# Performance work log

Measured on AMD Instinct MI355X. Metric: run time of the kernel, lower is better.

Reference implementation:

```python
import jax, jax.numpy as jnp
import numpy as np

B, T, D = 4, 1024, 1024
H, DH = 16, 64
SCALE = 1.0 / (DH ** 0.5)


def skew(QE):
    # QE: [B, H, T, 2T-1] -> relative-position skew (Music Transformer)
    b, h, t, _ = QE.shape
    QE = jnp.pad(QE, ((0, 0), (0, 0), (0, 0), (0, 1))).reshape(b, h, 2 * t * t)
    QE = jnp.pad(QE, ((0, 0), (0, 0), (0, t - 1))).reshape(b, h, t + 1, 2 * t - 1)
    return QE[:, :, :t, -t:]


def setup_inputs() -> dict:
    key = jax.random.key(0)
    ks = jax.random.split(key, 11)
    s = 0.02
    return {
        "x": jax.random.normal(ks[0], (B, T, D), jnp.float32),
        "context": jax.random.normal(ks[1], (B, T, D), jnp.float32),
        "mask": jax.random.randint(ks[2], (B, 1, T, T), 0, 2).astype(jnp.bool_),
        "lookup_table": jax.random.normal(ks[3], (2 * T - 1, DH), jnp.float32) * s,
        "Wq": jax.random.normal(ks[4], (D, H * DH), jnp.float32) * s,
        "Wk": jax.random.normal(ks[5], (D, H * DH), jnp.float32) * s,
        "Wv": jax.random.normal(ks[6], (D, H * DH), jnp.float32) * s,
        "Wo": jax.random.normal(ks[7], (H * DH, D), jnp.float32) * s,
        "bo": jnp.zeros((D,), jnp.float32),
        "gamma": jnp.ones((D,), jnp.float32),
        "beta": jnp.zeros((D,), jnp.float32),
    }


def reference(x, context, mask, lookup_table, Wq, Wk, Wv, Wo, bo, gamma, beta):
    b, t, d = x.shape
    # projections -> [B, H, T, DH]
    q = (x @ Wq).reshape(b, t, H, DH).transpose(0, 2, 1, 3)
    k = (context @ Wk).reshape(b, t, H, DH).transpose(0, 2, 1, 3)
    v = (context @ Wv).reshape(b, t, H, DH).transpose(0, 2, 1, 3)

    score = jnp.einsum("bhqd,bhkd->bhqk", q, k)
    score = score + skew(jnp.einsum("bhqd,rd->bhqr", q, lookup_table))
    score = score * SCALE
    score = jnp.where(mask, jnp.float32(-1e9), score)
    attn = jax.nn.softmax(score, axis=-1)

    out = jnp.einsum("bhqk,bhkd->bhqd", attn, v)
    out = out.transpose(0, 2, 1, 3).reshape(b, t, H * DH)
    out = out @ Wo + bo  # dropout is identity at inference (p effectively 0)

    y = x + out
    mu = jnp.mean(y, axis=-1, keepdims=True)
    var = jnp.var(y, axis=-1, keepdims=True)
    return (y - mu) / jnp.sqrt(var + 1e-5) * gamma + beta
```

## Files before the change

### kernel.cpp

```cpp
#include <hip/hip_runtime.h>

#define Tn 1024
#define Hn 16
#define Dn 1024
#define DHn 64
#define QSCALE 0.18033688011112042f

typedef unsigned short u16;
typedef unsigned long long ull;
typedef __bf16 bf16x8 __attribute__((ext_vector_type(8)));
typedef float f32x4 __attribute__((ext_vector_type(4)));

__device__ __forceinline__ u16 f2bf(float f) {
  union { float f; unsigned u; } v; v.f = f;
  return (u16)((v.u + 0x7FFFu + ((v.u >> 16) & 1u)) >> 16);
}
__device__ __forceinline__ float bf2f(u16 s) {
  union { unsigned u; float f; } v; v.u = ((unsigned)s) << 16;
  return v.f;
}
__device__ __forceinline__ f32x4 mfma16(bf16x8 a, bf16x8 b, f32x4 c) {
  return __builtin_amdgcn_mfma_f32_16x16x32_bf16(a, b, c, 0, 0, 0);
}

__global__ void k_convert(const float* __restrict__ src, u16* __restrict__ dst, int n) {
  int i = (blockIdx.x * blockDim.x + threadIdx.x) * 4;
  if (i >= n) return;
  float4 v = *(const float4*)(src + i);
  union { u16 s[4]; uint2 u; } o;
  o.s[0] = f2bf(v.x); o.s[1] = f2bf(v.y); o.s[2] = f2bf(v.z); o.s[3] = f2bf(v.w);
  *(uint2*)(dst + i) = o.u;
}

__global__ __launch_bounds__(256) void k_maskpack(const unsigned char* __restrict__ m,
                                                  unsigned long long* __restrict__ mb) {
  int wi = blockIdx.x * 4 + (threadIdx.x >> 6);
  int lane = threadIdx.x & 63;
  unsigned char v = m[((size_t)wi << 6) + lane];
  unsigned long long bal = __ballot(v != 0);
  if (lane == 0) mb[wi] = bal;
}

__global__ void k_transpose_convert(const float* __restrict__ W, u16* __restrict__ Wt) {
  __shared__ float tile[32][33];
  int n0 = blockIdx.x * 32, k0 = blockIdx.y * 32;
  int tx = threadIdx.x, ty = threadIdx.y;
  #pragma unroll
  for (int i = 0; i < 4; i++)
    tile[ty + 8*i][tx] = W[(size_t)(k0 + ty + 8*i) * Dn + n0 + tx];
  __syncthreads();
  #pragma unroll
  for (int i = 0; i < 4; i++)
    Wt[(size_t)(n0 + ty + 8*i) * Dn + k0 + tx] = f2bf(tile[tx][ty + 8*i]);
}

__global__ __launch_bounds__(256) void k_proj(const float* __restrict__ x, const float* __restrict__ ctxI,
                                              const u16* __restrict__ WqT, const u16* __restrict__ WkvT,
                                              u16* __restrict__ Qb, u16* __restrict__ Kb, u16* __restrict__ Vb) {
  __shared__ __align__(16) u16 Al[128][40];
  __shared__ __align__(16) u16 Bl[128][40];
  int bx = blockIdx.x;
  bool isQ = bx < 256;
  int idx = isQ ? bx : bx - 256;
  int m0 = (idx & 31) * 128;
  int n0 = (idx >> 5) * 128;
  const float* A = isQ ? x : ctxI;
  const u16* Bt = isQ ? WqT : WkvT;
  u16* dst0 = isQ ? Qb : Kb;
  float scale = isQ ? QSCALE : 1.0f;
  int tid = threadIdx.x;
  int w = tid >> 6, lane = tid & 63, g = lane >> 4, lr = lane & 15;
  int wr = w >> 1, wc = w & 1;
  f32x4 acc[4][4] = {};
  int sr = tid >> 2, sc = tid & 3;
  const float* Ap0 = &A[(size_t)(m0 + sr) * Dn + sc * 8];
  const float* Ap1 = Ap0 + (size_t)64 * Dn;
  const u16* Bp0 = &Bt[(size_t)(n0 + sr) * Dn + sc * 8];
  const u16* Bp1 = Bp0 + (size_t)64 * Dn;
  float4 ra0a = *(const float4*)Ap0, ra0b = *(const float4*)(Ap0 + 4);
  float4 ra1a = *(const float4*)Ap1, ra1b = *(const float4*)(Ap1 + 4);
  int4 rb0 = *(const int4*)Bp0;
  int4 rb1 = *(const int4*)Bp1;
  for (int k0 = 0; k0 < Dn; k0 += 32) {
    __syncthreads();
    {
      union { u16 s[8]; int4 v; } c0, c1;
      c0.s[0]=f2bf(ra0a.x); c0.s[1]=f2bf(ra0a.y); c0.s[2]=f2bf(ra0a.z); c0.s[3]=f2bf(ra0a.w);
      c0.s[4]=f2bf(ra0b.x); c0.s[5]=f2bf(ra0b.y); c0.s[6]=f2bf(ra0b.z); c0.s[7]=f2bf(ra0b.w);
      c1.s[0]=f2bf(ra1a.x); c1.s[1]=f2bf(ra1a.y); c1.s[2]=f2bf(ra1a.z); c1.s[3]=f2bf(ra1a.w);
      c1.s[4]=f2bf(ra1b.x); c1.s[5]=f2bf(ra1b.y); c1.s[6]=f2bf(ra1b.z); c1.s[7]=f2bf(ra1b.w);
      *(int4*)&Al[sr][sc*8]      = c0.v;
      *(int4*)&Al[sr + 64][sc*8] = c1.v;
    }
    *(int4*)&Bl[sr][sc*8]      = rb0;
    *(int4*)&Bl[sr + 64][sc*8] = rb1;
    __syncthreads();
    if (k0 + 32 < Dn) {
      ra0a = *(const float4*)(Ap0 + k0 + 32); ra0b = *(const float4*)(Ap0 + k0 + 36);
      ra1a = *(const float4*)(Ap1 + k0 + 32); ra1b = *(const float4*)(Ap1 + k0 + 36);
      rb0 = *(const int4*)(Bp0 + k0 + 32);
      rb1 = *(const int4*)(Bp1 + k0 + 32);
    }
    bf16x8 a[4], b[4];
    #pragma unroll
    for (int mi = 0; mi < 4; mi++) a[mi] = *(const bf16x8*)&Al[wr*64 + mi*16 + lr][g*8];
    #pragma unroll
    for (int ni = 0; ni < 4; ni++) b[ni] = *(const bf16x8*)&Bl[wc*64 + ni*16 + lr][g*8];
    #pragma unroll
    for (int mi = 0; mi < 4; mi++)
      #pragma unroll
      for (int ni = 0; ni < 4; ni++)
        acc[mi][ni] = mfma16(a[mi], b[ni], acc[mi][ni]);
  }
  #pragma unroll
  for (int mi = 0; mi < 4; mi++)
    #pragma unroll
    for (int ni = 0; ni < 4; ni++) {
      int row0 = m0 + wr*64 + mi*16 + g*4;
      int col = n0 + wc*64 + ni*16 + lr;
      int bb = row0 >> 10, tt0 = row0 & 1023;
      int hh = col >> 6, dd = col & 63;
      if (hh < 16) {
        u16* p = dst0 + (((size_t)(bb*16 + hh) << 10) + (size_t)tt0) * 64 + dd;
        #pragma unroll
        for (int r = 0; r < 4; r++) p[(size_t)r * 64] = f2bf(acc[mi][ni][r] * scale);
      } else {
        union { u16 s[4]; uint2 u; } o;
        #pragma unroll
        for (int r = 0; r < 4; r++) o.s[r] = f2bf(acc[mi][ni][r]);
        *(uint2*)(Vb + (((size_t)((bb*16 + (hh - 16)) * 64 + dd)) << 10) + tt0) = o.u;
      }
    }
}

__global__ __launch_bounds__(256) void k_gemm_bt(const u16* __restrict__ A, const u16* __restrict__ Bt,
                                                 u16* __restrict__ dst0, const float* __restrict__ bias) {
  __shared__ __align__(16) u16 Al[128][40];
  __shared__ __align__(16) u16 Bl[128][40];
  int m0 = blockIdx.y * 128, n0 = blockIdx.x * 128;
  int tid = threadIdx.x;
  int w = tid >> 6, lane = tid & 63, g = lane >> 4, lr = lane & 15;
  int wr = w >> 1, wc = w & 1;
  f32x4 acc[4][4] = {};
  int sr = tid >> 2, sc = tid & 3;
  const u16* Ap0 = &A[(size_t)(m0 + sr) * Dn + sc * 8];
  const u16* Ap1 = &A[(size_t)(m0 + sr + 64) * Dn + sc * 8];
  const u16* Bp0 = &Bt[(size_t)(n0 + sr) * Dn + sc * 8];
  const u16* Bp1 = &Bt[(size_t)(n0 + sr + 64) * Dn + sc * 8];
  int4 ra0 = *(const int4*)Ap0;
  int4 ra1 = *(const int4*)Ap1;
  int4 rb0 = *(const int4*)Bp0;
  int4 rb1 = *(const int4*)Bp1;
  for (int k0 = 0; k0 < Dn; k0 += 32) {
    __syncthreads();
    *(int4*)&Al[sr][sc*8]      = ra0;
    *(int4*)&Al[sr + 64][sc*8] = ra1;
    *(int4*)&Bl[sr][sc*8]      = rb0;
    *(int4*)&Bl[sr + 64][sc*8] = rb1;
    __syncthreads();
    if (k0 + 32 < Dn) {
      ra0 = *(const int4*)(Ap0 + k0 + 32);
      ra1 = *(const int4*)(Ap1 + k0 + 32);
      rb0 = *(const int4*)(Bp0 + k0 + 32);
      rb1 = *(const int4*)(Bp1 + k0 + 32);
    }
    bf16x8 a[4], b[4];
    #pragma unroll
    for (int mi = 0; mi < 4; mi++) a[mi] = *(const bf16x8*)&Al[wr*64 + mi*16 + lr][g*8];
    #pragma unroll
    for (int ni = 0; ni < 4; ni++) b[ni] = *(const bf16x8*)&Bl[wc*64 + ni*16 + lr][g*8];
    #pragma unroll
    for (int mi = 0; mi < 4; mi++)
      #pragma unroll
      for (int ni = 0; ni < 4; ni++)
        acc[mi][ni] = mfma16(a[mi], b[ni], acc[mi][ni]);
  }
  #pragma unroll
  for (int mi = 0; mi < 4; mi++)
    #pragma unroll
    for (int ni = 0; ni < 4; ni++) {
      int row0 = m0 + wr*64 + mi*16 + g*4;
      int col = n0 + wc*64 + ni*16 + lr;
      #pragma unroll
      for (int r = 0; r < 4; r++)
        dst0[(size_t)(row0 + r) * Dn + col] = f2bf(acc[mi][ni][r] + bias[col]);
    }
}

__global__ __launch_bounds__(512, 2) void k_attn(const u16* __restrict__ Qb, const u16* __restrict__ Kb,
                                              const u16* __restrict__ VT, const u16* __restrict__ Eb,
                                              const unsigned long long* __restrict__ mbits,
                                              u16* __restrict__ ctx) {
  __shared__ __align__(16) u16 KlF[128 * 64];
  __shared__ __align__(16) u16 Vt[64][136];
  __shared__ __align__(16) u16 RP[8][16][72];
  int h = blockIdx.y;
  int b = blockIdx.x;
  int q0 = blockIdx.z * 128;
  int tid = threadIdx.x;
  int w = tid >> 6, lane = tid & 63, g = lane >> 4, lr = lane & 15;
  int qw0 = q0 + w * 16;
  size_t headoff = (size_t)(b * Hn + h) * Tn * DHn;
  bf16x8 qf0 = *(const bf16x8*)&Qb[headoff + (size_t)(qw0 + lr)*64 + g*8];
  bf16x8 qf1 = *(const bf16x8*)&Qb[headoff + (size_t)(qw0 + lr)*64 + 32 + g*8];
  f32x4 O[4] = {};
  f32x4 Os = {0.f, 0.f, 0.f, 0.f};
  union { u16 s[8]; bf16x8 v; } one8;
  #pragma unroll
  for (int j = 0; j < 8; j++) one8.s[j] = 0x3F80u;

  int srcl[4]; bool psel[4];
  #pragma unroll
  for (int r = 0; r < 4; r++) {
    int rowq = g*4 + r;
    srcl[r] = (lane & 48) + ((lr - rowq + 15) & 15);
    psel[r] = (lr <= rowq);
  }
  const unsigned long long* mrow = mbits + ((size_t)(b * Tn + qw0 + g*4) << 4);

  f32x4 carry = {0.f, 0.f, 0.f, 0.f};
  {
    int rmin0 = 0 - qw0 + 1008;
    const u16* ep = &Eb[(size_t)(rmin0 + lr) * 64 + g*8];
    carry = mfma16(qf0, *(const bf16x8*)ep, carry);
    carry = mfma16(qf1, *(const bf16x8*)(ep + 32), carry);
  }

  int sKr = tid >> 3, sKc = (tid & 7) * 8;
  int kswz = sKc ^ ((sKr & 7) << 3);
  int sVr = tid >> 4, sVc = (tid & 15) * 8;
  const u16* Kgs = Kb + headoff + (size_t)sKr * 64 + sKc;
  const u16* Vgs = VT + headoff + (size_t)sVr * 1024 + sVc;
  int4 kA = *(const int4*)Kgs;
  int4 kB = *(const int4*)(Kgs + (size_t)64 * 64);
  int4 vA = *(const int4*)Vgs;
  int4 vB = *(const int4*)(Vgs + 32 * 1024);

  int kread = (g * 8) ^ ((lr & 7) << 3);
  int kread2 = (32 + g * 8) ^ ((lr & 7) << 3);

  for (int k0 = 0; k0 < Tn; k0 += 128) {
    __syncthreads();
    *(int4*)&KlF[sKr * 64 + kswz]        = kA;
    *(int4*)&KlF[(sKr + 64) * 64 + kswz] = kB;
    *(int4*)&Vt[sVr][sVc]                = vA;
    *(int4*)&Vt[sVr + 32][sVc]           = vB;
    __syncthreads();

    uint2 mw[2][4];
    #pragma unroll
    for (int t = 0; t < 2; t++)
      #pragma unroll
      for (int r = 0; r < 4; r++)
        mw[t][r] = *(const uint2*)(mrow + (size_t)r * 16 + (k0 >> 6) + t);

    int rmin0 = k0 - qw0 + 1008;
    bf16x8 pa00, pa01, pa10, pa11;

    f32x4 Rm0[5];
    Rm0[0] = carry;
    __builtin_amdgcn_s_setprio(1);
    #pragma unroll
    for (int jt = 1; jt < 5; jt++) {
      const u16* ep = &Eb[(size_t)(rmin0 + jt*16 + lr) * 64 + g*8];
      f32x4 R = {0.f, 0.f, 0.f, 0.f};
      R = mfma16(qf0, *(const bf16x8*)ep, R);
      R = mfma16(qf1, *(const bf16x8*)(ep + 32), R);
      Rm0[jt] = R;
    }
    f32x4 S0[4];
    #pragma unroll
    for (int c = 0; c < 4; c++) {
      int krow = c*16 + lr;
      f32x4 z = {0.f, 0.f, 0.f, 0.f};
      z = mfma16(qf0, *(const bf16x8*)&KlF[krow*64 + kread], z);
      z = mfma16(qf1, *(const bf16x8*)&KlF[krow*64 + kread2], z);
      S0[c] = z;
    }
    __builtin_amdgcn_s_setprio(0);
    {
      float sh[5][4];
      #pragma unroll
      for (int s5 = 0; s5 < 5; s5++)
        #pragma unroll
        for (int r = 0; r < 4; r++)
          sh[s5][r] = __shfl(Rm0[s5][r], srcl[r], 64);
      #pragma unroll
      for (int c = 0; c < 4; c++)
        #pragma unroll
        for (int r = 0; r < 4; r++) {
          float s = S0[c][r] + (psel[r] ? sh[c][r] : sh[c+1][r]);
          unsigned bit;
          if (c == 0)      bit = (mw[0][r].x >> lr) & 1u;
          else if (c == 1) bit = (mw[0][r].x >> (16 + lr)) & 1u;
          else if (c == 2) bit = (mw[0][r].y >> lr) & 1u;
          else             bit = (mw[0][r].y >> (16 + lr)) & 1u;
          s = bit ? -1e9f : s;
          RP[w][g*4 + r][c*16 + lr] = f2bf(__builtin_amdgcn_exp2f(s));
        }
      pa00 = *(const bf16x8*)&RP[w][lr][g*8];
      pa01 = *(const bf16x8*)&RP[w][lr][32 + g*8];
    }

    f32x4 Rm1[5];
    Rm1[0] = Rm0[4];
    __builtin_amdgcn_s_setprio(1);
    #pragma unroll
    for (int jt = 1; jt < 5; jt++) {
      const u16* ep = &Eb[(size_t)(rmin0 + 64 + jt*16 + lr) * 64 + g*8];
      f32x4 R = {0.f, 0.f, 0.f, 0.f};
      R = mfma16(qf0, *(const bf16x8*)ep, R);
      R = mfma16(qf1, *(const bf16x8*)(ep + 32), R);
      Rm1[jt] = R;
    }
    __builtin_amdgcn_s_setprio(0);
    carry = Rm1[4];

    __builtin_amdgcn_sched_barrier(0);
    if (k0 + 128 < Tn) {
      kA = *(const int4*)(Kgs + (size_t)(k0 + 128) * 64);
      kB = *(const int4*)(Kgs + (size_t)(k0 + 192) * 64);
      vA = *(const int4*)(Vgs + k0 + 128);
      vB = *(const int4*)(Vgs + 32 * 1024 + k0 + 128);
    }
    __builtin_amdgcn_sched_barrier(0);

    f32x4 S1[4];
    __builtin_amdgcn_s_setprio(1);
    #pragma unroll
    for (int c = 0; c < 4; c++) {
      int krow = 64 + c*16 + lr;
      f32x4 z = {0.f, 0.f, 0.f, 0.f};
      z = mfma16(qf0, *(const bf16x8*)&KlF[krow*64 + kread], z);
      z = mfma16(qf1, *(const bf16x8*)&KlF[krow*64 + kread2], z);
      S1[c] = z;
    }
    __builtin_amdgcn_s_setprio(0);
    {
      float sh[5][4];
      #pragma unroll
      for (int s5 = 0; s5 < 5; s5++)
        #pragma unroll
        for (int r = 0; r < 4; r++)
          sh[s5][r] = __shfl(Rm1[s5][r], srcl[r], 64);
      #pragma unroll
      for (int c = 0; c < 4; c++)
        #pragma unroll
        for (int r = 0; r < 4; r++) {
          float s = S1[c][r] + (psel[r] ? sh[c][r] : sh[c+1][r]);
          unsigned bit;
          if (c == 0)      bit = (mw[1][r].x >> lr) & 1u;
          else if (c == 1) bit = (mw[1][r].x >> (16 + lr)) & 1u;
          else if (c == 2) bit = (mw[1][r].y >> lr) & 1u;
          else             bit = (mw[1][r].y >> (16 + lr)) & 1u;
          s = bit ? -1e9f : s;
          RP[w][g*4 + r][c*16 + lr] = f2bf(__builtin_amdgcn_exp2f(s));
        }
      pa10 = *(const bf16x8*)&RP[w][lr][g*8];
      pa11 = *(const bf16x8*)&RP[w][lr][32 + g*8];
    }

    __builtin_amdgcn_s_setprio(1);
    #pragma unroll
    for (int ct = 0; ct < 4; ct++) {
      bf16x8 vf0 = *(const bf16x8*)&Vt[ct*16 + lr][g*8];
      bf16x8 vf1 = *(const bf16x8*)&Vt[ct*16 + lr][32 + g*8];
      O[ct] = mfma16(pa00, vf0, O[ct]);
      O[ct] = mfma16(pa01, vf1, O[ct]);
      bf16x8 vf2 = *(const bf16x8*)&Vt[ct*16 + lr][64 + g*8];
      bf16x8 vf3 = *(const bf16x8*)&Vt[ct*16 + lr][96 + g*8];
      O[ct] = mfma16(pa10, vf2, O[ct]);
      O[ct] = mfma16(pa11, vf3, O[ct]);
    }
    Os = mfma16(pa00, one8.v, Os);
    Os = mfma16(pa01, one8.v, Os);
    Os = mfma16(pa10, one8.v, Os);
    Os = mfma16(pa11, one8.v, Os);
    __builtin_amdgcn_s_setprio(0);
  }
  float inv[4];
  #pragma unroll
  for (int r = 0; r < 4; r++) inv[r] = 1.f / Os[r];
  #pragma unroll
  for (int ct = 0; ct < 4; ct++)
    #pragma unroll
    for (int r = 0; r < 4; r++) {
      int rowq = g*4 + r, col = ct*16 + lr;
      ctx[(size_t)(b*Tn + qw0 + rowq) * 1024 + h*64 + col] = f2bf(O[ct][r] * inv[r]);
    }
}

__global__ __launch_bounds__(256) void k_ln(const float* __restrict__ x, const u16* __restrict__ o,
                                            const float* __restrict__ gamma, const float* __restrict__ beta,
                                            float* __restrict__ out) {
  int m = blockIdx.x, tid = threadIdx.x;
  int w = tid >> 6, lane = tid & 63;
  const float* xr = x + (size_t)m * Dn;
  const u16* orow = o + (size_t)m * Dn;
  float4 xv = *(const float4*)&xr[tid*4];
  union { uint2 u; u16 s[4]; } ou;
  ou.u = *(const uint2*)&orow[tid*4];
  float y[4];
  y[0] = xv.x + bf2f(ou.s[0]);
  y[1] = xv.y + bf2f(ou.s[1]);
  y[2] = xv.z + bf2f(ou.s[2]);
  y[3] = xv.w + bf2f(ou.s[3]);
  float s = y[0]+y[1]+y[2]+y[3];
  float s2 = y[0]*y[0]+y[1]*y[1]+y[2]*y[2]+y[3]*y[3];
  #pragma unroll
  for (int off = 1; off < 64; off <<= 1) { s += __shfl_xor(s, off); s2 += __shfl_xor(s2, off); }
  __shared__ float red[8];
  if (lane == 0) { red[w] = s; red[4 + w] = s2; }
  __syncthreads();
  float Sa = red[0]+red[1]+red[2]+red[3];
  float Sb = red[4]+red[5]+red[6]+red[7];
  float mu = Sa * (1.f/1024.f);
  float var = Sb * (1.f/1024.f) - mu*mu;
  float rstd = rsqrtf(var + 1e-5f);
  #pragma unroll
  for (int i = 0; i < 4; i++) {
    int j = tid*4 + i;
    out[(size_t)m*Dn + j] = (y[i] - mu) * rstd * gamma[j] + beta[j];
  }
}

extern "C" void kernel_launch(void* const* d_in, const int* in_sizes, int n_in,
                              void* d_out, int out_size, void* d_ws, size_t ws_size,
                              hipStream_t stream) {
  const float* x    = (const float*)d_in[0];
  const float* ctxI = (const float*)d_in[1];
  const unsigned char* mask = (const unsigned char*)d_in[2];
  const float* lut  = (const float*)d_in[3];
  const float* Wq   = (const float*)d_in[4];
  const float* Wk   = (const float*)d_in[5];
  const float* Wv   = (const float*)d_in[6];
  const float* Wo   = (const float*)d_in[7];
  const float* bo   = (const float*)d_in[8];
  const float* gamma= (const float*)d_in[9];
  const float* beta = (const float*)d_in[10];
  float* out = (float*)d_out;

  u16* WqT  = (u16*)d_ws;
  u16* WkT  = WqT + 1048576;
  u16* WvT  = WkT + 1048576;
  u16* WoT  = WvT + 1048576;
  u16* Ebf  = WoT + 1048576;
  u16* Qbf  = Ebf + 131072;
  u16* Kbf  = Qbf + 4194304;
  u16* Vbf  = Kbf + 4194304;
  u16* ctxb = Vbf + 4194304;
  u16* obf  = ctxb + 4194304;
  unsigned long long* mbits = (unsigned long long*)(obf + 4194304);

  k_maskpack<<<16384, 256, 0, stream>>>(mask, mbits);
  k_convert<<<128, 256, 0, stream>>>(lut, Ebf, 131008);
  dim3 tb(32, 8), tg(32, 32);
  k_transpose_convert<<<tg, tb, 0, stream>>>(Wq, WqT);
  k_transpose_convert<<<tg, tb, 0, stream>>>(Wk, WkT);
  k_transpose_convert<<<tg, tb, 0, stream>>>(Wv, WvT);
  k_transpose_convert<<<tg, tb, 0, stream>>>(Wo, WoT);
  k_proj<<<768, 256, 0, stream>>>(x, ctxI, WqT, WkT, Qbf, Kbf, Vbf);
  k_attn<<<dim3(4, 16, 8), 512, 0, stream>>>(Qbf, Kbf, Vbf, Ebf, mbits, ctxb);
  k_gemm_bt<<<dim3(8, 32), 256, 0, stream>>>(ctxb, WoT, obf, bo);
  k_ln<<<4096, 256, 0, stream>>>(x, obf, gamma, beta, out);
}
```

Measured before the change: 189.5 us.

## Process two 16-row query tiles per wave in attention kernel

Each wave now handles 32 query rows instead of 16, so each block covers 256 queries and the grid halves along the query dimension. Every K/V tile staged in shared memory and every relative-position table fragment is reused across both row groups; the second group reuses the first group's E fragments shifted by one 16-row step. The aim is to cut shared-memory staging and global E loads per unit of work. In exchange, register pressure roughly doubles under launch_bounds(512,2), and only 256 blocks launch, which can leave compute units underoccupied.

```diff
diff --git a/kernel.cpp b/kernel.cpp
--- a/kernel.cpp
+++ b/kernel.cpp
@@ -196,15 +196,17 @@
   __shared__ __align__(16) u16 RP[8][16][72];
   int h = blockIdx.y;
   int b = blockIdx.x;
-  int q0 = blockIdx.z * 128;
+  int q0 = blockIdx.z * 256;
   int tid = threadIdx.x;
   int w = tid >> 6, lane = tid & 63, g = lane >> 4, lr = lane & 15;
-  int qw0 = q0 + w * 16;
+  int qw0 = q0 + w * 32;
   size_t headoff = (size_t)(b * Hn + h) * Tn * DHn;
   bf16x8 qf0 = *(const bf16x8*)&Qb[headoff + (size_t)(qw0 + lr)*64 + g*8];
   bf16x8 qf1 = *(const bf16x8*)&Qb[headoff + (size_t)(qw0 + lr)*64 + 32 + g*8];
-  f32x4 O[4] = {};
-  f32x4 Os = {0.f, 0.f, 0.f, 0.f};
+  bf16x8 qf2 = *(const bf16x8*)&Qb[headoff + (size_t)(qw0 + 16 + lr)*64 + g*8];
+  bf16x8 qf3 = *(const bf16x8*)&Qb[headoff + (size_t)(qw0 + 16 + lr)*64 + 32 + g*8];
+  f32x4 O[8] = {};
+  f32x4 Os0 = {0.f, 0.f, 0.f, 0.f}, Os1 = {0.f, 0.f, 0.f, 0.f};
   union { u16 s[8]; bf16x8 v; } one8;
   #pragma unroll
   for (int j = 0; j < 8; j++) one8.s[j] = 0x3F80u;
@@ -218,12 +220,15 @@
   }
   const unsigned long long* mrow = mbits + ((size_t)(b * Tn + qw0 + g*4) << 4);
 
-  f32x4 carry = {0.f, 0.f, 0.f, 0.f};
+  f32x4 carry0 = {0.f, 0.f, 0.f, 0.f}, carry1 = {0.f, 0.f, 0.f, 0.f};
   {
-    int rmin0 = 0 - qw0 + 1008;
-    const u16* ep = &Eb[(size_t)(rmin0 + lr) * 64 + g*8];
-    carry = mfma16(qf0, *(const bf16x8*)ep, carry);
-    carry = mfma16(qf1, *(const bf16x8*)(ep + 32), carry);
+    int rm = 1008 - qw0;
+    const u16* ep = &Eb[(size_t)(rm + lr) * 64 + g*8];
+    carry0 = mfma16(qf0, *(const bf16x8*)ep, carry0);
+    carry0 = mfma16(qf1, *(const bf16x8*)(ep + 32), carry0);
+    const u16* ep1 = &Eb[(size_t)(rm - 16 + lr) * 64 + g*8];
+    carry1 = mfma16(qf2, *(const bf16x8*)ep1, carry1);
+    carry1 = mfma16(qf3, *(const bf16x8*)(ep1 + 32), carry1);
   }
 
   int sKr = tid >> 3, sKc = (tid & 7) * 8;
@@ -247,74 +252,121 @@
     *(int4*)&Vt[sVr + 32][sVc]           = vB;
     __syncthreads();
 
-    uint2 mw[2][4];
+    uint2 mw0[2][4], mw1[2][4];
     #pragma unroll
     for (int t = 0; t < 2; t++)
       #pragma unroll
-      for (int r = 0; r < 4; r++)
-        mw[t][r] = *(const uint2*)(mrow + (size_t)r * 16 + (k0 >> 6) + t);
+      for (int r = 0; r < 4; r++) {
+        mw0[t][r] = *(const uint2*)(mrow + (size_t)r * 16 + (k0 >> 6) + t);
+        mw1[t][r] = *(const uint2*)(mrow + 256 + (size_t)r * 16 + (k0 >> 6) + t);
+      }
 
     int rmin0 = k0 - qw0 + 1008;
-    bf16x8 pa00, pa01, pa10, pa11;
-
-    f32x4 Rm0[5];
-    Rm0[0] = carry;
+    bf16x8 pa000, pa001, pa010, pa011;
+    bf16x8 pa100, pa101, pa110, pa111;
+
+    bf16x8 e0[5][2];
+    #pragma unroll
+    for (int j = 0; j < 5; j++) {
+      const u16* ep = &Eb[(size_t)(rmin0 + j*16 + lr) * 64 + g*8];
+      e0[j][0] = *(const bf16x8*)ep;
+      e0[j][1] = *(const bf16x8*)(ep + 32);
+    }
+    f32x4 Rm0[5], Rn0[5];
+    Rm0[0] = carry0;
+    Rn0[0] = carry1;
     __builtin_amdgcn_s_setprio(1);
     #pragma unroll
-    for (int jt = 1; jt < 5; jt++) {
-      const u16* ep = &Eb[(size_t)(rmin0 + jt*16 + lr) * 64 + g*8];
+    for (int j = 1; j < 5; j++) {
       f32x4 R = {0.f, 0.f, 0.f, 0.f};
-      R = mfma16(qf0, *(const bf16x8*)ep, R);
-      R = mfma16(qf1, *(const bf16x8*)(ep + 32), R);
-      Rm0[jt] = R;
-    }
-    f32x4 S0[4];
+      R = mfma16(qf0, e0[j][0], R);
+      R = mfma16(qf1, e0[j][1], R);
+      Rm0[j] = R;
+      f32x4 R2 = {0.f, 0.f, 0.f, 0.f};
+      R2 = mfma16(qf2, e0[j-1][0], R2);
+      R2 = mfma16(qf3, e0[j-1][1], R2);
+      Rn0[j] = R2;
+    }
+    f32x4 S0[4], T0[4];
     #pragma unroll
     for (int c = 0; c < 4; c++) {
       int krow = c*16 + lr;
+      bf16x8 kf0 = *(const bf16x8*)&KlF[krow*64 + kread];
+      bf16x8 kf1 = *(const bf16x8*)&KlF[krow*64 + kread2];
       f32x4 z = {0.f, 0.f, 0.f, 0.f};
-      z = mfma16(qf0, *(const bf16x8*)&KlF[krow*64 + kread], z);
-      z = mfma16(qf1, *(const bf16x8*)&KlF[krow*64 + kread2], z);
+      z = mfma16(qf0, kf0, z); z = mfma16(qf1, kf1, z);
       S0[c] = z;
+      f32x4 z2 = {0.f, 0.f, 0.f, 0.f};
+      z2 = mfma16(qf2, kf0, z2); z2 = mfma16(qf3, kf1, z2);
+      T0[c] = z2;
     }
     __builtin_amdgcn_s_setprio(0);
     {
-      float sh[5][4];
+      float sh[5][4], si[5][4];
       #pragma unroll
       for (int s5 = 0; s5 < 5; s5++)
         #pragma unroll
-        for (int r = 0; r < 4; r++)
+        for (int r = 0; r < 4; r++) {
           sh[s5][r] = __shfl(Rm0[s5][r], srcl[r], 64);
+          si[s5][r] = __shfl(Rn0[s5][r], srcl[r], 64);
+        }
       #pragma unroll
       for (int c = 0; c < 4; c++)
         #pragma unroll
         for (int r = 0; r < 4; r++) {
           float s = S0[c][r] + (psel[r] ? sh[c][r] : sh[c+1][r]);
           unsigned bit;
-          if (c == 0)      bit = (mw[0][r].x >> lr) & 1u;
-          else if (c == 1) bit = (mw[0][r].x >> (16 + lr)) & 1u;
-          else if (c == 2) bit = (mw[0][r].y >> lr) & 1u;
-          else             bit = (mw[0][r].y >> (16 + lr)) & 1u;
+          if (c == 0)      bit = (mw0[0][r].x >> lr) & 1u;
+          else if (c == 1) bit = (mw0[0][r].x >> (16 + lr)) & 1u;
+          else if (c == 2) bit = (mw0[0][r].y >> lr) & 1u;
+          else             bit = (mw0[0][r].y >> (16 + lr)) & 1u;
           s = bit ? -1e9f : s;
           RP[w][g*4 + r][c*16 + lr] = f2bf(__builtin_amdgcn_exp2f(s));
         }
-      pa00 = *(const bf16x8*)&RP[w][lr][g*8];
-      pa01 = *(const bf16x8*)&RP[w][lr][32 + g*8];
-    }
-
-    f32x4 Rm1[5];
+      pa000 = *(const bf16x8*)&RP[w][lr][g*8];
+      pa001 = *(const bf16x8*)&RP[w][lr][32 + g*8];
+      #pragma unroll
+      for (int c = 0; c < 4; c++)
+        #pragma unroll
+        for (int r = 0; r < 4; r++) {
+          float s = T0[c][r] + (psel[r] ? si[c][r] : si[c+1][r]);
+          unsigned bit;
+          if (c == 0)      bit = (mw1[0][r].x >> lr) & 1u;
+          else if (c == 1) bit = (mw1[0][r].x >> (16 + lr)) & 1u;
+          else if (c == 2) bit = (mw1[0][r].y >> lr) & 1u;
+          else             bit = (mw1[0][r].y >> (16 + lr)) & 1u;
+          s = bit ? -1e9f : s;
+          RP[w][g*4 + r][c*16 + lr] = f2bf(__builtin_amdgcn_exp2f(s));
+        }
+      pa010 = *(const bf16x8*)&RP[w][lr][g*8];
+      pa011 = *(const bf16x8*)&RP[w][lr][32 + g*8];
+    }
+
+    bf16x8 e1[5][2];
+    #pragma unroll
+    for (int j = 0; j < 5; j++) {
+      const u16* ep = &Eb[(size_t)(rmin0 + 64 + j*16 + lr) * 64 + g*8];
+      e1[j][0] = *(const bf16x8*)ep;
+      e1[j][1] = *(const bf16x8*)(ep + 32);
+    }
+    f32x4 Rm1[5], Rn1[5];
     Rm1[0] = Rm0[4];
+    Rn1[0] = Rn0[4];
     __builtin_amdgcn_s_setprio(1);
     #pragma unroll
-    for (int jt = 1; jt < 5; jt++) {
-      const u16* ep = &Eb[(size_t)(rmin0 + 64 + jt*16 + lr) * 64 + g*8];
+    for (int j = 1; j < 5; j++) {
       f32x4 R = {0.f, 0.f, 0.f, 0.f};
-      R = mfma16(qf0, *(const bf16x8*)ep, R);
-      R = mfma16(qf1, *(const bf16x8*)(ep + 32), R);
-      Rm1[jt] = R;
+      R = mfma16(qf0, e1[j][0], R);
+      R = mfma16(qf1, e1[j][1], R);
+      Rm1[j] = R;
+      f32x4 R2 = {0.f, 0.f, 0.f, 0.f};
+      R2 = mfma16(qf2, e1[j-1][0], R2);
+      R2 = mfma16(qf3, e1[j-1][1], R2);
+      Rn1[j] = R2;
     }
     __builtin_amdgcn_s_setprio(0);
-    carry = Rm1[4];
+    carry0 = Rm1[4];
+    carry1 = Rn1[4];
 
     __builtin_amdgcn_sched_barrier(0);
     if (k0 + 128 < Tn) {
@@ -325,39 +377,60 @@
     }
     __builtin_amdgcn_sched_barrier(0);
 
-    f32x4 S1[4];
+    f32x4 S1[4], T1[4];
     __builtin_amdgcn_s_setprio(1);
     #pragma unroll
     for (int c = 0; c < 4; c++) {
       int krow = 64 + c*16 + lr;
+      bf16x8 kf0 = *(const bf16x8*)&KlF[krow*64 + kread];
+      bf16x8 kf1 = *(const bf16x8*)&KlF[krow*64 + kread2];
       f32x4 z = {0.f, 0.f, 0.f, 0.f};
-      z = mfma16(qf0, *(const bf16x8*)&KlF[krow*64 + kread], z);
-      z = mfma16(qf1, *(const bf16x8*)&KlF[krow*64 + kread2], z);
+      z = mfma16(qf0, kf0, z); z = mfma16(qf1, kf1, z);
       S1[c] = z;
+      f32x4 z2 = {0.f, 0.f, 0.f, 0.f};
+      z2 = mfma16(qf2, kf0, z2); z2 = mfma16(qf3, kf1, z2);
+      T1[c] = z2;
     }
     __builtin_amdgcn_s_setprio(0);
     {
-      float sh[5][4];
+      float sh[5][4], si[5][4];
       #pragma unroll
       for (int s5 = 0; s5 < 5; s5++)
         #pragma unroll
-        for (int r = 0; r < 4; r++)
+        for (int r = 0; r < 4; r++) {
           sh[s5][r] = __shfl(Rm1[s5][r], srcl[r], 64);
+          si[s5][r] = __shfl(Rn1[s5][r], srcl[r], 64);
+        }
       #pragma unroll
       for (int c = 0; c < 4; c++)
         #pragma unroll
         for (int r = 0; r < 4; r++) {
           float s = S1[c][r] + (psel[r] ? sh[c][r] : sh[c+1][r]);
           unsigned bit;
-          if (c == 0)      bit = (mw[1][r].x >> lr) & 1u;
-          else if (c == 1) bit = (mw[1][r].x >> (16 + lr)) & 1u;
-          else if (c == 2) bit = (mw[1][r].y >> lr) & 1u;
-          else             bit = (mw[1][r].y >> (16 + lr)) & 1u;
+          if (c == 0)      bit = (mw0[1][r].x >> lr) & 1u;
+          else if (c == 1) bit = (mw0[1][r].x >> (16 + lr)) & 1u;
+          else if (c == 2) bit = (mw0[1][r].y >> lr) & 1u;
+          else             bit = (mw0[1][r].y >> (16 + lr)) & 1u;
           s = bit ? -1e9f : s;
           RP[w][g*4 + r][c*16 + lr] = f2bf(__builtin_amdgcn_exp2f(s));
         }
-      pa10 = *(const bf16x8*)&RP[w][lr][g*8];
-      pa11 = *(const bf16x8*)&RP[w][lr][32 + g*8];
+      pa100 = *(const bf16x8*)&RP[w][lr][g*8];
+      pa101 = *(const bf16x8*)&RP[w][lr][32 + g*8];
+      #pragma unroll
+      for (int c = 0; c < 4; c++)
+        #pragma unroll
+        for (int r = 0; r < 4; r++) {
+          float s = T1[c][r] + (psel[r] ? si[c][r] : si[c+1][r]);
+          unsigned bit;
+          if (c == 0)      bit = (mw1[1][r].x >> lr) & 1u;
+          else if (c == 1) bit = (mw1[1][r].x >> (16 + lr)) & 1u;
+          else if (c == 2) bit = (mw1[1][r].y >> lr) & 1u;
+          else             bit = (mw1[1][r].y >> (16 + lr)) & 1u;
+          s = bit ? -1e9f : s;
+          RP[w][g*4 + r][c*16 + lr] = f2bf(__builtin_amdgcn_exp2f(s));
+        }
+      pa110 = *(const bf16x8*)&RP[w][lr][g*8];
+      pa111 = *(const bf16x8*)&RP[w][lr][32 + g*8];
     }
 
     __builtin_amdgcn_s_setprio(1);
@@ -365,28 +438,37 @@
     for (int ct = 0; ct < 4; ct++) {
       bf16x8 vf0 = *(const bf16x8*)&Vt[ct*16 + lr][g*8];
       bf16x8 vf1 = *(const bf16x8*)&Vt[ct*16 + lr][32 + g*8];
-      O[ct] = mfma16(pa00, vf0, O[ct]);
-      O[ct] = mfma16(pa01, vf1, O[ct]);
       bf16x8 vf2 = *(const bf16x8*)&Vt[ct*16 + lr][64 + g*8];
       bf16x8 vf3 = *(const bf16x8*)&Vt[ct*16 + lr][96 + g*8];
-      O[ct] = mfma16(pa10, vf2, O[ct]);
-      O[ct] = mfma16(pa11, vf3, O[ct]);
-    }
-    Os = mfma16(pa00, one8.v, Os);
-    Os = mfma16(pa01, one8.v, Os);
-    Os = mfma16(pa10, one8.v, Os);
-    Os = mfma16(pa11, one8.v, Os);
+      O[ct] = mfma16(pa000, vf0, O[ct]);
+      O[ct] = mfma16(pa001, vf1, O[ct]);
+      O[ct] = mfma16(pa100, vf2, O[ct]);
+      O[ct] = mfma16(pa101, vf3, O[ct]);
+      O[4+ct] = mfma16(pa010, vf0, O[4+ct]);
+      O[4+ct] = mfma16(pa011, vf1, O[4+ct]);
+      O[4+ct] = mfma16(pa110, vf2, O[4+ct]);
+      O[4+ct] = mfma16(pa111, vf3, O[4+ct]);
+    }
+    Os0 = mfma16(pa000, one8.v, Os0);
+    Os0 = mfma16(pa001, one8.v, Os0);
+    Os0 = mfma16(pa100, one8.v, Os0);
+    Os0 = mfma16(pa101, one8.v, Os0);
+    Os1 = mfma16(pa010, one8.v, Os1);
+    Os1 = mfma16(pa011, one8.v, Os1);
+    Os1 = mfma16(pa110, one8.v, Os1);
+    Os1 = mfma16(pa111, one8.v, Os1);
     __builtin_amdgcn_s_setprio(0);
   }
-  float inv[4];
-  #pragma unroll
-  for (int r = 0; r < 4; r++) inv[r] = 1.f / Os[r];
+  float inv0[4], inv1[4];
+  #pragma unroll
+  for (int r = 0; r < 4; r++) { inv0[r] = 1.f / Os0[r]; inv1[r] = 1.f / Os1[r]; }
   #pragma unroll
   for (int ct = 0; ct < 4; ct++)
     #pragma unroll
     for (int r = 0; r < 4; r++) {
       int rowq = g*4 + r, col = ct*16 + lr;
-      ctx[(size_t)(b*Tn + qw0 + rowq) * 1024 + h*64 + col] = f2bf(O[ct][r] * inv[r]);
+      ctx[(size_t)(b*Tn + qw0 + rowq) * 1024 + h*64 + col] = f2bf(O[ct][r] * inv0[r]);
+      ctx[(size_t)(b*Tn + qw0 + 16 + rowq) * 1024 + h*64 + col] = f2bf(O[4+ct][r] * inv1[r]);
     }
 }
 
@@ -460,7 +542,7 @@
   k_transpose_convert<<<tg, tb, 0, stream>>>(Wv, WvT);
   k_transpose_convert<<<tg, tb, 0, stream>>>(Wo, WoT);
   k_proj<<<768, 256, 0, stream>>>(x, ctxI, WqT, WkT, Qbf, Kbf, Vbf);
-  k_attn<<<dim3(4, 16, 8), 512, 0, stream>>>(Qbf, Kbf, Vbf, Ebf, mbits, ctxb);
+  k_attn<<<dim3(4, 16, 4), 512, 0, stream>>>(Qbf, Kbf, Vbf, Ebf, mbits, ctxb);
   k_gemm_bt<<<dim3(8, 32), 256, 0, stream>>>(ctxb, WoT, obf, bo);
   k_ln<<<4096, 256, 0, stream>>>(x, obf, gamma, beta, out);
 }
```

New measurement: 164.7 us. 1.15x faster.
